# Kernel optimization log

Measured on AMD Instinct MI355X. Metric: run time of the kernel, lower is better.

Reference implementation:

```python
import jax, jax.numpy as jnp
import numpy as np


def setup_inputs() -> dict:
    key = jax.random.key(0)
    k1, k2, k3, k4 = jax.random.split(key, 4)
    B, n, f, k = 32768, 512, 30, 40
    X = jax.random.normal(k1, (B, n), dtype=jnp.float32)
    w1 = jax.random.normal(k2, (n, 1), dtype=jnp.float32) * 0.01
    b = jnp.zeros((1,), dtype=jnp.float32)
    v = jax.random.normal(k3, (n, f, k), dtype=jnp.float32) * 0.01
    feature2field = jax.random.randint(k4, (n,), 0, f, dtype=jnp.int32)
    return {"X": X, "w1": w1, "b": b, "v": v, "feature2field": feature2field}


def reference(X, w1, b, v, feature2field):
    # linear terms: [B]
    linear = (X @ w1).reshape(-1) + b[0]
    n = v.shape[0]
    # A[i, j] = v[i, feature2field[j]]  -> [n, n, k]
    A = v[:, feature2field, :]
    # pair coefficient C[i, j] = sum_k v[i, field[j], k] * v[j, field[i], k]
    C = jnp.einsum('ijk,jik->ij', A, A)
    # strict upper triangle matches the i<j loop in the original
    Cm = C * jnp.triu(jnp.ones((n, n), dtype=C.dtype), k=1)
    # interaction[b] = sum_{i<j} C[i,j] * X[b,i] * X[b,j]
    inter = jnp.einsum('bi,ij,bj->b', X, Cm, X)
    logits = linear + inter
    return jax.nn.sigmoid(logits)
```

## Files before the change

kernel.cpp:

```cpp
#include <hip/hip_runtime.h>
#include <hip/hip_bf16.h>
#include <math.h>


#define N_FEAT 512
#define FK 1200
#define KDIM 40
#define B_ROWS 32768
#define BM 128
#define NSTEP 16

typedef __attribute__((ext_vector_type(8))) short short8;
typedef __attribute__((ext_vector_type(16))) float f32x16;

__device__ __forceinline__ unsigned short bf16_rne(float f) {
    union { float f; unsigned int u; } c; c.f = f;
    unsigned int u = c.u;
    u += 0x7fffu + ((u >> 16) & 1u);
    return (unsigned short)(u >> 16);
}

__device__ __forceinline__ float bf16_to_f(unsigned short h) {
    union { unsigned int u; float f; } c;
    c.u = ((unsigned int)h) << 16;
    return c.f;
}

__global__ __launch_bounds__(256) void build_wpk(const float* __restrict__ v,
                                                 const int* __restrict__ f2f,
                                                 unsigned short* __restrict__ Wpk) {
    __shared__ float a_lds[FK];
    __shared__ float c_lds[256 * 44];

    const int i   = blockIdx.y;
    const int j0  = blockIdx.x * 256;
    const int tid = threadIdx.x;
    const int fi  = f2f[i];

    for (int q = tid; q < FK; q += 256) a_lds[q] = v[(size_t)i * FK + q];
    for (int q = tid; q < 2560; q += 256) {
        const int jl = q / 10, c4 = q % 10;
        *(float4*)&c_lds[jl * 44 + c4 * 4] =
            *(const float4*)&v[(size_t)(j0 + jl) * FK + fi * KDIM + c4 * 4];
    }
    __syncthreads();

    const int j  = j0 + tid;
    const int fj = f2f[j];
    const float4* a = (const float4*)&a_lds[fj * KDIM];
    const float4* c = (const float4*)&c_lds[tid * 44];
    float acc = 0.f;
#pragma unroll
    for (int q = 0; q < KDIM / 4; ++q) {
        float4 av = a[q], cv = c[q];
        acc = fmaf(av.x, cv.x, acc);
        acc = fmaf(av.y, cv.y, acc);
        acc = fmaf(av.z, cv.z, acc);
        acc = fmaf(av.w, cv.w, acc);
    }
    const unsigned short val = (i == j) ? (unsigned short)0 : bf16_rne(0.5f * acc);
    Wpk[((size_t)(j >> 3) * 512 + i) * 8 + (j & 7)] = val;
}

__global__ __launch_bounds__(512, 1) void ffm_fused(const float* __restrict__ X,
                                                    const unsigned short* __restrict__ Wpk,
                                                    const float* __restrict__ w1,
                                                    const float* __restrict__ bvec,
                                                    float* __restrict__ out) {
    __shared__ __align__(16) unsigned short As[BM * N_FEAT];
    __shared__ float part[4 * BM];

    const int tid  = threadIdx.x;
    const int lane = tid & 63;
    const int wave = tid >> 6;
    const int half = lane >> 5;
    const int l31  = lane & 31;
    const int wm   = wave & 1;
    const int wn   = wave >> 1;

    const size_t row0 = (size_t)blockIdx.x * BM;

    const unsigned short* wp = Wpk + ((size_t)half * 512 + wn * 128 + l31) * 8;

    {
        const float4* X4 = (const float4*)(X + row0 * N_FEAT);
#pragma unroll 2
        for (int u = 0; u < 16; ++u) {
            const int g  = u * 512 + tid;
            const int r  = g >> 6;
            const int kc = g & 63;
            float4 f0 = X4[r * 128 + kc * 2];
            float4 f1 = X4[r * 128 + kc * 2 + 1];
            union { unsigned short us[8]; short8 v; } pk;
            pk.us[0] = bf16_rne(f0.x);
            pk.us[1] = bf16_rne(f0.y);
            pk.us[2] = bf16_rne(f0.z);
            pk.us[3] = bf16_rne(f0.w);
            pk.us[4] = bf16_rne(f1.x);
            pk.us[5] = bf16_rne(f1.y);
            pk.us[6] = bf16_rne(f1.z);
            pk.us[7] = bf16_rne(f1.w);
            *(short8*)(As + ((size_t)kc * BM + (r ^ (kc & 7))) * 8) = pk.v;
        }
    }
    asm volatile("s_waitcnt lgkmcnt(0)" ::: "memory");
    __builtin_amdgcn_s_barrier();

    f32x16 acc[2][4];
#pragma unroll
    for (int mi = 0; mi < 2; ++mi)
#pragma unroll
        for (int ci = 0; ci < 4; ++ci)
#pragma unroll
            for (int r = 0; r < 16; ++r) acc[mi][ci][r] = 0.f;

    short8 fb[2][2][4];
    short8 fa[2][2][2];

#pragma unroll
    for (int si = 0; si < 2; ++si)
#pragma unroll
        for (int ci = 0; ci < 4; ++ci) {
            fb[0][si][ci] = *(const short8*)(wp + ((size_t)((si * 2) * 512 + ci * 32)) * 8);
            fb[1][si][ci] = *(const short8*)(wp + ((size_t)((4 + si * 2) * 512 + ci * 32)) * 8);
        }
#pragma unroll
    for (int si = 0; si < 2; ++si) {
        const int kr = si * 2 + half;
#pragma unroll
        for (int mi = 0; mi < 2; ++mi) {
            const int row = wm * 64 + mi * 32 + l31;
            fa[0][si][mi] = *(const short8*)(As + ((size_t)kr * BM + (row ^ kr)) * 8);
        }
    }

    const unsigned short* wpt = wp;
    const unsigned short* at  = (const unsigned short*)As;

#pragma unroll 1
    for (int t = 0; t < 14; t += 2) {
#pragma unroll
        for (int si = 0; si < 2; ++si) {
            const int kr = 4 + si * 2 + half;
#pragma unroll
            for (int mi = 0; mi < 2; ++mi) {
                const int row = wm * 64 + mi * 32 + l31;
                fa[1][si][mi] = *(const short8*)(at + ((size_t)kr * BM + (row ^ (kr & 7))) * 8);
            }
        }
#pragma unroll
        for (int si = 0; si < 2; ++si)
#pragma unroll
            for (int mi = 0; mi < 2; ++mi)
#pragma unroll
                for (int ci = 0; ci < 4; ++ci)
                    acc[mi][ci] = __builtin_amdgcn_mfma_f32_32x32x16_bf16(
                        fa[0][si][mi], fb[0][si][ci], acc[mi][ci], 0, 0, 0);
#pragma unroll
        for (int si = 0; si < 2; ++si)
#pragma unroll
            for (int ci = 0; ci < 4; ++ci)
                fb[0][si][ci] = *(const short8*)(wpt +
                    ((size_t)((8 + si * 2) * 512 + ci * 32)) * 8);
#pragma unroll
        for (int si = 0; si < 2; ++si) {
            const int kr = 8 + si * 2 + half;
            const int ks = (si * 2 + half);
#pragma unroll
            for (int mi = 0; mi < 2; ++mi) {
                const int row = wm * 64 + mi * 32 + l31;
                fa[0][si][mi] = *(const short8*)(at + ((size_t)kr * BM + (row ^ ks)) * 8);
            }
        }
#pragma unroll
        for (int si = 0; si < 2; ++si)
#pragma unroll
            for (int mi = 0; mi < 2; ++mi)
#pragma unroll
                for (int ci = 0; ci < 4; ++ci)
                    acc[mi][ci] = __builtin_amdgcn_mfma_f32_32x32x16_bf16(
                        fa[1][si][mi], fb[1][si][ci], acc[mi][ci], 0, 0, 0);
#pragma unroll
        for (int si = 0; si < 2; ++si)
#pragma unroll
            for (int ci = 0; ci < 4; ++ci)
                fb[1][si][ci] = *(const short8*)(wpt +
                    ((size_t)((12 + si * 2) * 512 + ci * 32)) * 8);

        wpt += (size_t)8 * 512 * 8;
        at  += (size_t)8 * BM * 8;
    }

#pragma unroll
    for (int si = 0; si < 2; ++si) {
        const int kr = 4 + si * 2 + half;
#pragma unroll
        for (int mi = 0; mi < 2; ++mi) {
            const int row = wm * 64 + mi * 32 + l31;
            fa[1][si][mi] = *(const short8*)(at + ((size_t)kr * BM + (row ^ (kr & 7))) * 8);
        }
    }
#pragma unroll
    for (int si = 0; si < 2; ++si)
#pragma unroll
        for (int mi = 0; mi < 2; ++mi)
#pragma unroll
            for (int ci = 0; ci < 4; ++ci)
                acc[mi][ci] = __builtin_amdgcn_mfma_f32_32x32x16_bf16(
                    fa[0][si][mi], fb[0][si][ci], acc[mi][ci], 0, 0, 0);
#pragma unroll
    for (int si = 0; si < 2; ++si)
#pragma unroll
        for (int mi = 0; mi < 2; ++mi)
#pragma unroll
            for (int ci = 0; ci < 4; ++ci)
                acc[mi][ci] = __builtin_amdgcn_mfma_f32_32x32x16_bf16(
                    fa[1][si][mi], fb[1][si][ci], acc[mi][ci], 0, 0, 0);

    float w1v[4];
#pragma unroll
    for (int ci = 0; ci < 4; ++ci) w1v[ci] = w1[wn * 128 + ci * 32 + l31];
    const float bias = bvec[0];

    float rs[2][16];
#pragma unroll
    for (int mi = 0; mi < 2; ++mi) {
#pragma unroll
        for (int reg = 0; reg < 16; ++reg) {
            const int row = wm * 64 + mi * 32 + (reg & 3) + 8 * (reg >> 2) + 4 * half;
            float s = 0.f;
#pragma unroll
            for (int ci = 0; ci < 4; ++ci) {
                const int gc = wn * 128 + ci * 32 + l31;
                const int kc = gc >> 3;
                const float xf = bf16_to_f(As[((size_t)kc * BM + (row ^ (kc & 7))) * 8 + (gc & 7)]);
                s = fmaf(xf, acc[mi][ci][reg] + w1v[ci], s);
            }
            rs[mi][reg] = s;
        }
    }

#pragma unroll
    for (int mi = 0; mi < 2; ++mi)
#pragma unroll
        for (int reg = 0; reg < 16; ++reg) {
            float r = rs[mi][reg];
#pragma unroll
            for (int off = 1; off < 32; off <<= 1)
                r += __shfl_xor(r, off, 32);
            rs[mi][reg] = r;
        }
    if (l31 == 0) {
#pragma unroll
        for (int mi = 0; mi < 2; ++mi)
#pragma unroll
            for (int reg = 0; reg < 16; ++reg) {
                const int row = wm * 64 + mi * 32 + (reg & 3) + 8 * (reg >> 2) + 4 * half;
                part[wn * BM + row] = rs[mi][reg];
            }
    }
    __syncthreads();

    if (tid < BM) {
        float tsum = bias;
#pragma unroll
        for (int q = 0; q < 4; ++q) tsum += part[q * BM + tid];
        out[row0 + tid] = 1.0f / (1.0f + expf(-tsum));
    }
}

extern "C" void kernel_launch(void* const* d_in, const int* in_sizes, int n_in,
                              void* d_out, int out_size, void* d_ws, size_t ws_size,
                              hipStream_t stream) {
    const float* X   = (const float*)d_in[0];
    const float* w1  = (const float*)d_in[1];
    const float* b   = (const float*)d_in[2];
    const float* v   = (const float*)d_in[3];
    const int*   f2f = (const int*)d_in[4];
    float* out = (float*)d_out;

    unsigned short* Wpk = (unsigned short*)d_ws;

    build_wpk<<<dim3(2, N_FEAT), 256, 0, stream>>>(v, f2f, Wpk);
    ffm_fused<<<B_ROWS / BM, 512, 0, stream>>>(X, Wpk, w1, b, out);
}
```

Measured before the change: 127.5 us.

## Split X bf16 conversion into separate kernel and async-load pre-swizzled tiles

Adds a pre-pass kernel that converts X to bf16 and writes it in the swizzled LDS tile layout to workspace. A new GEMM kernel then fills shared memory with global_load_lds direct copies instead of converting on the fly. The intent is to take conversion work off the MFMA kernel's critical path and shorten the LDS fill. In exchange it adds an extra 32 MB write and read through HBM plus one more kernel launch, and it only runs when the workspace is large enough.

```diff
diff --git a/kernel.cpp b/kernel.cpp
--- a/kernel.cpp
+++ b/kernel.cpp
@@ -26,6 +26,13 @@
     return c.f;
 }
 
+__device__ __forceinline__ void async_copy16(const void* g, void* l) {
+    __builtin_amdgcn_global_load_lds(
+        (const __attribute__((address_space(1))) void*)g,
+        (__attribute__((address_space(3))) void*)l,
+        16, 0, 0);
+}
+
 __global__ __launch_bounds__(256) void build_wpk(const float* __restrict__ v,
                                                  const int* __restrict__ f2f,
                                                  unsigned short* __restrict__ Wpk) {
@@ -60,6 +67,245 @@
     }
     const unsigned short val = (i == j) ? (unsigned short)0 : bf16_rne(0.5f * acc);
     Wpk[((size_t)(j >> 3) * 512 + i) * 8 + (j & 7)] = val;
+}
+
+__global__ __launch_bounds__(512) void xconvert(const float* __restrict__ X,
+                                                unsigned short* __restrict__ Xbf) {
+    __shared__ __align__(16) unsigned short T[BM * N_FEAT];
+
+    const int tid = threadIdx.x;
+    const size_t row0 = (size_t)blockIdx.x * BM;
+    const float4* X4 = (const float4*)(X + row0 * N_FEAT);
+
+#pragma unroll
+    for (int h = 0; h < 2; ++h) {
+        float4 f[16];
+#pragma unroll
+        for (int i = 0; i < 8; ++i) {
+            const int g = (h * 8 + i) * 512 + tid;
+            const int r = g >> 6, kc = g & 63;
+            f[i * 2]     = X4[r * 128 + kc * 2];
+            f[i * 2 + 1] = X4[r * 128 + kc * 2 + 1];
+        }
+#pragma unroll
+        for (int i = 0; i < 8; ++i) {
+            const int g = (h * 8 + i) * 512 + tid;
+            const int r = g >> 6, kc = g & 63;
+            union { unsigned short us[8]; short8 v; } pk;
+            pk.us[0] = bf16_rne(f[i * 2].x);
+            pk.us[1] = bf16_rne(f[i * 2].y);
+            pk.us[2] = bf16_rne(f[i * 2].z);
+            pk.us[3] = bf16_rne(f[i * 2].w);
+            pk.us[4] = bf16_rne(f[i * 2 + 1].x);
+            pk.us[5] = bf16_rne(f[i * 2 + 1].y);
+            pk.us[6] = bf16_rne(f[i * 2 + 1].z);
+            pk.us[7] = bf16_rne(f[i * 2 + 1].w);
+            *(short8*)(T + ((size_t)kc * BM + (r ^ (kc & 7))) * 8) = pk.v;
+        }
+    }
+    __syncthreads();
+
+    unsigned short* dst = Xbf + (size_t)blockIdx.x * 8192 * 8;
+#pragma unroll
+    for (int i = 0; i < 16; ++i) {
+        const int u = i * 512 + tid;
+        *(short8*)(dst + (size_t)u * 8) = *(const short8*)(T + (size_t)u * 8);
+    }
+}
+
+__global__ __launch_bounds__(512, 1) void ffm_gemm(const unsigned short* __restrict__ Xbf,
+                                                   const unsigned short* __restrict__ Wpk,
+                                                   const float* __restrict__ w1,
+                                                   const float* __restrict__ bvec,
+                                                   float* __restrict__ out) {
+    __shared__ __align__(16) unsigned short As[BM * N_FEAT];
+    __shared__ float part[4 * BM];
+
+    const int tid  = threadIdx.x;
+    const int lane = tid & 63;
+    const int wave = tid >> 6;
+    const int half = lane >> 5;
+    const int l31  = lane & 31;
+    const int wm   = wave & 1;
+    const int wn   = wave >> 1;
+
+    const size_t row0 = (size_t)blockIdx.x * BM;
+
+    const unsigned short* wp = Wpk + ((size_t)half * 512 + wn * 128 + l31) * 8;
+
+    short8 fb[2][2][4];
+    short8 fa[2][2][2];
+
+#pragma unroll
+    for (int si = 0; si < 2; ++si)
+#pragma unroll
+        for (int ci = 0; ci < 4; ++ci) {
+            fb[0][si][ci] = *(const short8*)(wp + ((size_t)((si * 2) * 512 + ci * 32)) * 8);
+            fb[1][si][ci] = *(const short8*)(wp + ((size_t)((4 + si * 2) * 512 + ci * 32)) * 8);
+        }
+
+    {
+        const unsigned short* xsrc = Xbf + (size_t)blockIdx.x * 8192 * 8;
+#pragma unroll
+        for (int i = 0; i < 16; ++i) {
+            const int u = i * 512 + tid;
+            async_copy16(xsrc + (size_t)u * 8, (unsigned short*)As + (size_t)u * 8);
+        }
+    }
+    asm volatile("s_waitcnt vmcnt(0)" ::: "memory");
+    __builtin_amdgcn_s_barrier();
+
+    f32x16 acc[2][4];
+#pragma unroll
+    for (int mi = 0; mi < 2; ++mi)
+#pragma unroll
+        for (int ci = 0; ci < 4; ++ci)
+#pragma unroll
+            for (int r = 0; r < 16; ++r) acc[mi][ci][r] = 0.f;
+
+#pragma unroll
+    for (int si = 0; si < 2; ++si) {
+        const int kr = si * 2 + half;
+#pragma unroll
+        for (int mi = 0; mi < 2; ++mi) {
+            const int row = wm * 64 + mi * 32 + l31;
+            fa[0][si][mi] = *(const short8*)(As + ((size_t)kr * BM + (row ^ kr)) * 8);
+        }
+    }
+
+    const unsigned short* wpt = wp;
+    const unsigned short* at  = (const unsigned short*)As;
+
+#pragma unroll 1
+    for (int t = 0; t < 14; t += 2) {
+#pragma unroll
+        for (int si = 0; si < 2; ++si) {
+            const int kr = 4 + si * 2 + half;
+#pragma unroll
+            for (int mi = 0; mi < 2; ++mi) {
+                const int row = wm * 64 + mi * 32 + l31;
+                fa[1][si][mi] = *(const short8*)(at + ((size_t)kr * BM + (row ^ (kr & 7))) * 8);
+            }
+        }
+#pragma unroll
+        for (int si = 0; si < 2; ++si)
+#pragma unroll
+            for (int mi = 0; mi < 2; ++mi)
+#pragma unroll
+                for (int ci = 0; ci < 4; ++ci)
+                    acc[mi][ci] = __builtin_amdgcn_mfma_f32_32x32x16_bf16(
+                        fa[0][si][mi], fb[0][si][ci], acc[mi][ci], 0, 0, 0);
+#pragma unroll
+        for (int si = 0; si < 2; ++si)
+#pragma unroll
+            for (int ci = 0; ci < 4; ++ci)
+                fb[0][si][ci] = *(const short8*)(wpt +
+                    ((size_t)((8 + si * 2) * 512 + ci * 32)) * 8);
+#pragma unroll
+        for (int si = 0; si < 2; ++si) {
+            const int kr = 8 + si * 2 + half;
+            const int ks = (si * 2 + half);
+#pragma unroll
+            for (int mi = 0; mi < 2; ++mi) {
+                const int row = wm * 64 + mi * 32 + l31;
+                fa[0][si][mi] = *(const short8*)(at + ((size_t)kr * BM + (row ^ ks)) * 8);
+            }
+        }
+#pragma unroll
+        for (int si = 0; si < 2; ++si)
+#pragma unroll
+            for (int mi = 0; mi < 2; ++mi)
+#pragma unroll
+                for (int ci = 0; ci < 4; ++ci)
+                    acc[mi][ci] = __builtin_amdgcn_mfma_f32_32x32x16_bf16(
+                        fa[1][si][mi], fb[1][si][ci], acc[mi][ci], 0, 0, 0);
+#pragma unroll
+        for (int si = 0; si < 2; ++si)
+#pragma unroll
+            for (int ci = 0; ci < 4; ++ci)
+                fb[1][si][ci] = *(const short8*)(wpt +
+                    ((size_t)((12 + si * 2) * 512 + ci * 32)) * 8);
+
+        wpt += (size_t)8 * 512 * 8;
+        at  += (size_t)8 * BM * 8;
+    }
+
+#pragma unroll
+    for (int si = 0; si < 2; ++si) {
+        const int kr = 4 + si * 2 + half;
+#pragma unroll
+        for (int mi = 0; mi < 2; ++mi) {
+            const int row = wm * 64 + mi * 32 + l31;
+            fa[1][si][mi] = *(const short8*)(at + ((size_t)kr * BM + (row ^ (kr & 7))) * 8);
+        }
+    }
+#pragma unroll
+    for (int si = 0; si < 2; ++si)
+#pragma unroll
+        for (int mi = 0; mi < 2; ++mi)
+#pragma unroll
+            for (int ci = 0; ci < 4; ++ci)
+                acc[mi][ci] = __builtin_amdgcn_mfma_f32_32x32x16_bf16(
+                    fa[0][si][mi], fb[0][si][ci], acc[mi][ci], 0, 0, 0);
+#pragma unroll
+    for (int si = 0; si < 2; ++si)
+#pragma unroll
+        for (int mi = 0; mi < 2; ++mi)
+#pragma unroll
+            for (int ci = 0; ci < 4; ++ci)
+                acc[mi][ci] = __builtin_amdgcn_mfma_f32_32x32x16_bf16(
+                    fa[1][si][mi], fb[1][si][ci], acc[mi][ci], 0, 0, 0);
+
+    float w1v[4];
+#pragma unroll
+    for (int ci = 0; ci < 4; ++ci) w1v[ci] = w1[wn * 128 + ci * 32 + l31];
+    const float bias = bvec[0];
+
+    float rs[2][16];
+#pragma unroll
+    for (int mi = 0; mi < 2; ++mi) {
+#pragma unroll
+        for (int reg = 0; reg < 16; ++reg) {
+            const int row = wm * 64 + mi * 32 + (reg & 3) + 8 * (reg >> 2) + 4 * half;
+            float s = 0.f;
+#pragma unroll
+            for (int ci = 0; ci < 4; ++ci) {
+                const int gc = wn * 128 + ci * 32 + l31;
+                const int kc = gc >> 3;
+                const float xf = bf16_to_f(As[((size_t)kc * BM + (row ^ (kc & 7))) * 8 + (gc & 7)]);
+                s = fmaf(xf, acc[mi][ci][reg] + w1v[ci], s);
+            }
+            rs[mi][reg] = s;
+        }
+    }
+
+#pragma unroll
+    for (int mi = 0; mi < 2; ++mi)
+#pragma unroll
+        for (int reg = 0; reg < 16; ++reg) {
+            float r = rs[mi][reg];
+#pragma unroll
+            for (int off = 1; off < 32; off <<= 1)
+                r += __shfl_xor(r, off, 32);
+            rs[mi][reg] = r;
+        }
+    if (l31 == 0) {
+#pragma unroll
+        for (int mi = 0; mi < 2; ++mi)
+#pragma unroll
+            for (int reg = 0; reg < 16; ++reg) {
+                const int row = wm * 64 + mi * 32 + (reg & 3) + 8 * (reg >> 2) + 4 * half;
+                part[wn * BM + row] = rs[mi][reg];
+            }
+    }
+    __syncthreads();
+
+    if (tid < BM) {
+        float tsum = bias;
+#pragma unroll
+        for (int q = 0; q < 4; ++q) tsum += part[q * BM + tid];
+        out[row0 + tid] = 1.0f / (1.0f + expf(-tsum));
+    }
 }
 
 __global__ __launch_bounds__(512, 1) void ffm_fused(const float* __restrict__ X,
@@ -79,7 +325,6 @@
     const int wn   = wave >> 1;
 
     const size_t row0 = (size_t)blockIdx.x * BM;
-
     const unsigned short* wp = Wpk + ((size_t)half * 512 + wn * 128 + l31) * 8;
 
     {
@@ -282,5 +527,13 @@
     unsigned short* Wpk = (unsigned short*)d_ws;
 
     build_wpk<<<dim3(2, N_FEAT), 256, 0, stream>>>(v, f2f, Wpk);
-    ffm_fused<<<B_ROWS / BM, 512, 0, stream>>>(X, Wpk, w1, b, out);
-}
+
+    const size_t need = ((size_t)1 << 20) + ((size_t)32 << 20);
+    if (ws_size >= need) {
+        unsigned short* Xbf = (unsigned short*)((char*)d_ws + ((size_t)1 << 20));
+        xconvert<<<B_ROWS / BM, 512, 0, stream>>>(X, Xbf);
+        ffm_gemm<<<B_ROWS / BM, 512, 0, stream>>>(Xbf, Wpk, w1, b, out);
+    } else {
+        ffm_fused<<<B_ROWS / BM, 512, 0, stream>>>(X, Wpk, w1, b, out);
+    }
+}
```

Measured after the change: 138.6 us. +8.7%, slower.
